# Kernel optimization log

Measured on AMD Instinct MI355X. Metric: run time of the kernel, lower is better.

Reference implementation:

```python
import jax, jax.numpy as jnp
import numpy as np

N_NODES = 100000
N_EDGES = 1600000
N_FEAT = 128
HIDDEN = 128
N_GRAPHS = 100


def setup_inputs() -> dict:
    key = jax.random.key(0)
    ks = jax.random.split(key, 12)
    glorot = lambda k, fi, fo: jax.random.normal(k, (fo, fi), jnp.float32) * (1.0 / np.sqrt(fi))
    x = jax.random.normal(ks[0], (N_NODES, N_FEAT), jnp.float32)
    edge_index = jax.random.randint(ks[1], (2, N_EDGES), 0, N_NODES, jnp.int64)
    batch = jnp.sort(jax.random.randint(ks[2], (N_NODES,), 0, N_GRAPHS, jnp.int64))
    return {
        "x": x,
        "edge_index": edge_index,
        "batch": batch,
        "W1": glorot(ks[3], N_FEAT, HIDDEN), "b1": jnp.zeros((HIDDEN,), jnp.float32),
        "W2": glorot(ks[4], HIDDEN, HIDDEN), "b2": jnp.zeros((HIDDEN,), jnp.float32),
        "W3": glorot(ks[5], HIDDEN, HIDDEN), "b3": jnp.zeros((HIDDEN,), jnp.float32),
        "W4": glorot(ks[6], HIDDEN, HIDDEN), "b4": jnp.zeros((HIDDEN,), jnp.float32),
    }


def _aggregate(x, edge_index):
    # GIN aggregation with eps=0: (1+eps)*x_i + sum_{j in N(i)} x_j
    src, dst = edge_index[0], edge_index[1]
    agg = jax.ops.segment_sum(x[src], dst, num_segments=N_NODES)
    return x + agg


def _mlp(h, Wa, ba, Wb, bb):
    h = jax.nn.relu(h @ Wa.T + ba)
    return jax.nn.relu(h @ Wb.T + bb)


def reference(x, edge_index, batch, W1, b1, W2, b2, W3, b3, W4, b4):
    # conv1: GINConv(MLP1), then extra relu (no-op after MLP's relu), dropout in eval = identity
    h = _mlp(_aggregate(x, edge_index), W1, b1, W2, b2)
    # conv2: GINConv(MLP2), then relu
    h = _mlp(_aggregate(h, edge_index), W3, b3, W4, b4)
    # global mean pool over graphs
    sums = jax.ops.segment_sum(h, batch, num_segments=N_GRAPHS)
    counts = jax.ops.segment_sum(jnp.ones((h.shape[0],), h.dtype), batch, num_segments=N_GRAPHS)
    x_pool = sums / jnp.maximum(counts, 1.0)[:, None]
    return (x_pool, h)
```

## Files before the change

### kernel.cpp

```cpp
#include <hip/hip_runtime.h>

#define N_NODES  100000
#define N_EDGES  1600000
#define NF       128
#define N_GRAPHS 100
#define NBKT     391
#define BKT_SHIFT 8
#define CAP      6144
#define CAPN     48
#define EPB      2048
#define EB_GRID  782
#define MBLK64   1563

typedef __attribute__((ext_vector_type(8))) short bf16x8;
typedef __attribute__((ext_vector_type(4))) float f32x4;
typedef __attribute__((ext_vector_type(2))) float f32x2;
typedef unsigned int uint32;

__device__ __forceinline__ unsigned short f2bf(float f) {
    union { float f; uint32 u; } x; x.f = f;
    return (unsigned short)((x.u + 0x7fffu + ((x.u >> 16) & 1u)) >> 16);
}
__device__ __forceinline__ uint32 pack2bf(float a, float b) {
    union { float f; uint32 u; } x, y; x.f = a; y.f = b;
    uint32 lo = (x.u + 0x7fffu + ((x.u >> 16) & 1u)) >> 16;
    uint32 hi = (y.u + 0x7fffu + ((y.u >> 16) & 1u)) & 0xffff0000u;
    return lo | hi;
}
__device__ __forceinline__ void add8(f32x2* acc, uint4 u4) {
    uint32 u[4] = {u4.x, u4.y, u4.z, u4.w};
    #pragma unroll
    for (int i = 0; i < 4; ++i) {
        union { uint32 b; float f; } lo, hi;
        lo.b = u[i] << 16; hi.b = u[i] & 0xffff0000u;
        acc[i] += (f32x2){lo.f, hi.f};
    }
}

__global__ __launch_bounds__(256) void prep(const float4* __restrict__ x,
                                            const float4* __restrict__ w1,
                                            const float4* __restrict__ w2,
                                            const float4* __restrict__ w3,
                                            const float4* __restrict__ w4,
                                            uint4* __restrict__ xb, uint4* __restrict__ wb,
                                            int* __restrict__ cur, float* __restrict__ sums) {
    int bid = blockIdx.x, t = threadIdx.x;
    if (bid < 6250) {
        int i = bid * 256 + t;
        float4 a = x[i * 2], b = x[i * 2 + 1];
        uint4 o;
        o.x = pack2bf(a.x, a.y); o.y = pack2bf(a.z, a.w);
        o.z = pack2bf(b.x, b.y); o.w = pack2bf(b.z, b.w);
        xb[i] = o;
    } else if (bid < 6282) {
        int i = (bid - 6250) * 256 + t;
        int wi = i >> 11, li = i & 2047;
        const float4* s = (wi == 0) ? w1 : (wi == 1) ? w2 : (wi == 2) ? w3 : w4;
        float4 a = s[li * 2], b = s[li * 2 + 1];
        uint4 o;
        o.x = pack2bf(a.x, a.y); o.y = pack2bf(a.z, a.w);
        o.z = pack2bf(b.x, b.y); o.w = pack2bf(b.z, b.w);
        wb[i] = o;
    } else {
        int idx = (bid - 6282) * 256 + t;
        for (int i = idx; i < N_GRAPHS * NF; i += 4096) sums[i] = 0.f;
        if (idx < NBKT) cur[idx] = 0;
    }
}

__global__ __launch_bounds__(512) void bscatter(const int* __restrict__ src,
                                                const int* __restrict__ dst,
                                                int* __restrict__ cur,
                                                uint32* __restrict__ ebuf) {
    __shared__ int lh[NBKT], lbase[NBKT];
    int t = threadIdx.x;
    if (t < NBKT) lh[t] = 0;
    __syncthreads();
    int e0 = blockIdx.x * EPB;
    int d[4];
    #pragma unroll
    for (int i = 0; i < 4; ++i) {
        int e = e0 + i * 512 + t;
        d[i] = -1;
        if (e < N_EDGES) { d[i] = dst[e]; atomicAdd(&lh[d[i] >> BKT_SHIFT], 1); }
    }
    __syncthreads();
    if (t < NBKT) { lbase[t] = t * CAP + (lh[t] ? atomicAdd(&cur[t], lh[t]) : 0); lh[t] = 0; }
    __syncthreads();
    #pragma unroll
    for (int i = 0; i < 4; ++i) {
        int e = e0 + i * 512 + t;
        if (e < N_EDGES) {
            int b = d[i] >> BKT_SHIFT;
            int off = atomicAdd(&lh[b], 1);
            ebuf[lbase[b] + off] = ((uint32)(d[i] & 255) << 17) | (uint32)src[e];
        }
    }
}

__global__ __launch_bounds__(256) void bfine(const uint32* __restrict__ ebuf,
                                             const int* __restrict__ cur,
                                             int* __restrict__ cnt,
                                             int* __restrict__ csr) {
    __shared__ int off[256];
    __shared__ __align__(16) int lcsr[256 * CAPN];
    int t = threadIdx.x;
    int bkt = blockIdx.x;
    int beg = bkt * CAP;
    int end = beg + min(cur[bkt], CAP);
    off[t] = 0;
    __syncthreads();
    for (int e = beg + t; e < end; e += 256) {
        uint32 u = ebuf[e];
        int local = (int)(u >> 17);
        int pos = atomicAdd(&off[local], 1);
        if (pos < CAPN)
            lcsr[local * CAPN + pos] = (int)(u & 0x1FFFFu);
    }
    __syncthreads();
    int node = (bkt << BKT_SHIFT) + t;
    if (node < N_NODES) cnt[node] = min(off[t], CAPN);
    uint4* dstq = (uint4*)(csr + (size_t)bkt * 256 * CAPN);
    const uint4* srcq = (const uint4*)lcsr;
    for (int i = t; i < 256 * CAPN / 4; i += 256)
        dstq[i] = srcq[i];
}

__global__ __launch_bounds__(256) void gather_agg_bf16(const uint4* __restrict__ x,
                                                       const int* __restrict__ cnt,
                                                       const int* __restrict__ csr,
                                                       uint4* __restrict__ out) {
    int gid  = blockIdx.x * 256 + threadIdx.x;
    int node = gid >> 6;
    int l = threadIdx.x & 63;
    int c = l & 15;
    int j = l >> 4;
    int beg = node * CAPN;

    uint4 vself = x[(size_t)node * 16 + c];
    int myE = csr[beg + min(l, CAPN - 1)];
    int deg = cnt[node];

    f32x2 acc[4];
    #pragma unroll
    for (int i = 0; i < 4; ++i) acc[i] = (f32x2){0.f, 0.f};

    uint4 v[8];
    int ok[8];
    #pragma unroll
    for (int k = 0; k < 4; ++k) {
        int sl = j + 4 * k;
        int sle = max(min(sl, deg - 1), 0);
        unsigned s = (unsigned)__shfl(myE, sle, 64);
        s = min(s, (unsigned)(N_NODES - 1));
        v[k] = x[(size_t)s * 16 + c];
        ok[k] = sl < deg;
    }
    if (deg > 16) {
        #pragma unroll
        for (int k = 0; k < 4; ++k) {
            int sl = 16 + j + 4 * k;
            int sle = min(sl, deg - 1);
            unsigned s = (unsigned)__shfl(myE, sle, 64);
            s = min(s, (unsigned)(N_NODES - 1));
            v[4 + k] = x[(size_t)s * 16 + c];
            ok[4 + k] = sl < deg;
        }
    }
    #pragma unroll
    for (int k = 0; k < 4; ++k) if (ok[k]) add8(acc, v[k]);
    if (deg > 16) {
        #pragma unroll
        for (int k = 0; k < 4; ++k) if (ok[4 + k]) add8(acc, v[4 + k]);
        for (int sl0 = 32; sl0 < deg; sl0 += 16) {
            #pragma unroll
            for (int k = 0; k < 4; ++k) {
                int sl = sl0 + j + 4 * k;
                int sle = min(sl, deg - 1);
                unsigned s = (unsigned)__shfl(myE, sle, 64);
                s = min(s, (unsigned)(N_NODES - 1));
                uint4 vv = x[(size_t)s * 16 + c];
                if (sl < deg) add8(acc, vv);
            }
        }
    }

    #pragma unroll
    for (int i = 0; i < 4; ++i) {
        acc[i].x += __shfl_xor(acc[i].x, 16, 64);
        acc[i].y += __shfl_xor(acc[i].y, 16, 64);
        acc[i].x += __shfl_xor(acc[i].x, 32, 64);
        acc[i].y += __shfl_xor(acc[i].y, 32, 64);
    }

    add8(acc, vself);

    if (j == 0) {
        uint4 o;
        o.x = pack2bf(acc[0].x, acc[0].y); o.y = pack2bf(acc[1].x, acc[1].y);
        o.z = pack2bf(acc[2].x, acc[2].y); o.w = pack2bf(acc[3].x, acc[3].y);
        out[(size_t)node * 16 + c] = o;
    }
}

template <bool F32OUT, bool POOL>
__global__ __launch_bounds__(256, 8) void mlp64(const unsigned short* __restrict__ A,
                                                const unsigned short* __restrict__ Wa,
                                                const float* __restrict__ ba,
                                                const unsigned short* __restrict__ Wb,
                                                const float* __restrict__ bb,
                                                void* __restrict__ Cout,
                                                const int* __restrict__ batch,
                                                float* __restrict__ sums) {
    __shared__ __align__(16) unsigned short Mid[64 * 136];
    int tid = threadIdx.x;
    int wv = tid >> 6, l = tid & 63, lm = l & 15, q = l >> 4;
    int row0  = blockIdx.x * 64;
    int trow0 = row0 + wv * 16;

    const unsigned short* pa  = A + (size_t)min(trow0 + lm, N_NODES - 1) * NF;
    const unsigned short* pwa = Wa + lm * NF;
    const unsigned short* pwb = Wb + lm * NF;

    f32x4 acc[8];
    #pragma unroll
    for (int ct = 0; ct < 8; ++ct) acc[ct] = (f32x4){0.f, 0.f, 0.f, 0.f};

    #pragma unroll
    for (int ks = 0; ks < 4; ++ks) {
        int ko = ks * 32 + q * 8;
        bf16x8 a = *(const bf16x8*)(pa + ko);
        #pragma unroll
        for (int ct = 0; ct < 8; ++ct) {
            bf16x8 b = *(const bf16x8*)(pwa + ct * 16 * NF + ko);
            acc[ct] = __builtin_amdgcn_mfma_f32_16x16x32_bf16(a, b, acc[ct], 0, 0, 0);
        }
    }

    #pragma unroll
    for (int ct = 0; ct < 8; ++ct) {
        int col = ct * 16 + lm;
        float bv = ba[col];
        #pragma unroll
        for (int r = 0; r < 4; ++r) {
            int rr = wv * 16 + q * 4 + r;
            Mid[rr * 136 + col] = f2bf(fmaxf(acc[ct][r] + bv, 0.f));
        }
    }
    __syncthreads();

    #pragma unroll
    for (int ct = 0; ct < 8; ++ct) acc[ct] = (f32x4){0.f, 0.f, 0.f, 0.f};

    const unsigned short* pm = &Mid[(wv * 16 + lm) * 136];
    #pragma unroll
    for (int ks = 0; ks < 4; ++ks) {
        int ko = ks * 32 + q * 8;
        bf16x8 a = *(const bf16x8*)(pm + ko);
        #pragma unroll
        for (int ct = 0; ct < 8; ++ct) {
            bf16x8 b = *(const bf16x8*)(pwb + ct * 16 * NF + ko);
            acc[ct] = __builtin_amdgcn_mfma_f32_16x16x32_bf16(a, b, acc[ct], 0, 0, 0);
        }
    }

    int gr[4];
    bool uni = true;
    if (POOL) {
        int gA = batch[min(trow0,      N_NODES - 1)];
        int gB = batch[min(trow0 + 15, N_NODES - 1)];
        uni = (gA == gB);
        gr[0] = gA;
        if (!uni) {
            #pragma unroll
            for (int r = 0; r < 4; ++r)
                gr[r] = batch[min(trow0 + q * 4 + r, N_NODES - 1)];
        }
    }

    #pragma unroll
    for (int ct = 0; ct < 8; ++ct) {
        int col = ct * 16 + lm;
        float bv = bb[col];
        float ps = 0.f;
        #pragma unroll
        for (int r = 0; r < 4; ++r) {
            int row = trow0 + q * 4 + r;
            if (row < N_NODES) {
                float vv = fmaxf(acc[ct][r] + bv, 0.f);
                if (F32OUT) ((float*)Cout)[(size_t)row * NF + col] = vv;
                else ((unsigned short*)Cout)[(size_t)row * NF + col] = f2bf(vv);
                if (POOL) {
                    if (uni) ps += vv;
                    else atomicAdd(&sums[gr[r] * NF + col], vv);
                }
            }
        }
        if (POOL && uni) {
            ps += __shfl_xor(ps, 16, 64);
            ps += __shfl_xor(ps, 32, 64);
            if (q == 0) atomicAdd(&sums[gr[0] * NF + col], ps);
        }
    }
}

__global__ __launch_bounds__(256) void pool_div2(const float* __restrict__ sums,
                                                 const int* __restrict__ batch,
                                                 float* __restrict__ out) {
    int i = blockIdx.x * 256 + threadIdx.x;
    if (i >= N_GRAPHS * NF) return;
    int g = i >> 7;
    int lo = 0, hi = N_NODES;
    while (lo < hi) { int m = (lo + hi) >> 1; if (batch[m] < g) lo = m + 1; else hi = m; }
    int lo2 = lo, hi2 = N_NODES;
    while (lo2 < hi2) { int m = (lo2 + hi2) >> 1; if (batch[m] < g + 1) lo2 = m + 1; else hi2 = m; }
    float cnt = (float)(lo2 - lo);
    out[i] = sums[i] / fmaxf(cnt, 1.f);
}

extern "C" void kernel_launch(void* const* d_in, const int* in_sizes, int n_in,
                              void* d_out, int out_size, void* d_ws, size_t ws_size,
                              hipStream_t stream) {
    const float* x     = (const float*)d_in[0];
    const int*   ei    = (const int*)d_in[1];
    const int*   batch = (const int*)d_in[2];
    const float* W1 = (const float*)d_in[3];  const float* b1 = (const float*)d_in[4];
    const float* W2 = (const float*)d_in[5];  const float* b2 = (const float*)d_in[6];
    const float* W3 = (const float*)d_in[7];  const float* b3 = (const float*)d_in[8];
    const float* W4 = (const float*)d_in[9];  const float* b4 = (const float*)d_in[10];
    const int* src = ei;
    const int* dst = ei + N_EDGES;

    float* out   = (float*)d_out;
    float* h_out = out + N_GRAPHS * NF;

    const size_t NE = (size_t)N_NODES * NF;
    unsigned short* xb = (unsigned short*)d_ws;
    unsigned short* t0 = xb + NE;
    unsigned short* t1 = t0 + NE;
    unsigned short* Wb = t1 + NE;
    int*    csr  = (int*)(Wb + 4 * NF * NF);
    int*    cntp = csr + (size_t)NBKT * 256 * CAPN;
    int*    curp = cntp + N_NODES;
    float*  sums = (float*)(curp + NBKT);
    uint32* ebuf = (uint32*)t1;

    const int gather_blocks = N_NODES * 64 / 256;

    prep<<<6250 + 32 + 16, 256, 0, stream>>>((const float4*)x,
                                             (const float4*)W1, (const float4*)W2,
                                             (const float4*)W3, (const float4*)W4,
                                             (uint4*)xb, (uint4*)Wb, curp, sums);

    bscatter<<<EB_GRID, 512, 0, stream>>>(src, dst, curp, ebuf);
    bfine<<<NBKT, 256, 0, stream>>>(ebuf, curp, cntp, csr);

    gather_agg_bf16<<<gather_blocks, 256, 0, stream>>>((const uint4*)xb, cntp, csr, (uint4*)t0);
    mlp64<false, false><<<MBLK64, 256, 0, stream>>>(t0, Wb + 0 * NF * NF, b1,
                                                    Wb + 1 * NF * NF, b2, t1, batch, sums);

    gather_agg_bf16<<<gather_blocks, 256, 0, stream>>>((const uint4*)t1, cntp, csr, (uint4*)t0);
    mlp64<true, true><<<MBLK64, 256, 0, stream>>>(t0, Wb + 2 * NF * NF, b3,
                                                  Wb + 3 * NF * NF, b4, h_out, batch, sums);

    pool_div2<<<(N_GRAPHS * NF + 255) / 256, 256, 0, stream>>>(sums, batch, out);
}
```

Measured before the change: 439.4 us.

## Double MLP row tile to 128 and stage outputs through LDS for coalesced stores

The fused two-layer MLP kernel now processes 128 rows per block: each wave computes two 16-row tiles and reuses each weight fragment load across both. The epilogue writes results into shared memory and then emits coalesced 16-byte row stores, instead of scattered per-element 2- or 4-byte stores. The fp32 output path is staged in two halves to fit in LDS. Costs are more registers and LDS, launch bounds reduced to 4 blocks, half as many blocks, and extra barriers.

```diff
diff --git a/kernel.cpp b/kernel.cpp
--- a/kernel.cpp
+++ b/kernel.cpp
@@ -10,7 +10,7 @@
 #define CAPN     48
 #define EPB      2048
 #define EB_GRID  782
-#define MBLK64   1563
+#define MBLK     782
 
 typedef __attribute__((ext_vector_type(8))) short bf16x8;
 typedef __attribute__((ext_vector_type(4))) float f32x4;
@@ -204,102 +204,153 @@
 }
 
 template <bool F32OUT, bool POOL>
-__global__ __launch_bounds__(256, 8) void mlp64(const unsigned short* __restrict__ A,
-                                                const unsigned short* __restrict__ Wa,
-                                                const float* __restrict__ ba,
-                                                const unsigned short* __restrict__ Wb,
-                                                const float* __restrict__ bb,
-                                                void* __restrict__ Cout,
-                                                const int* __restrict__ batch,
-                                                float* __restrict__ sums) {
-    __shared__ __align__(16) unsigned short Mid[64 * 136];
-    int tid = threadIdx.x;
+__global__ __launch_bounds__(256, 4) void mlp_mfma(const unsigned short* __restrict__ A,
+                                                   const unsigned short* __restrict__ Wa,
+                                                   const float* __restrict__ ba,
+                                                   const unsigned short* __restrict__ Wb,
+                                                   const float* __restrict__ bb,
+                                                   void* __restrict__ Cout,
+                                                   const int* __restrict__ batch,
+                                                   float* __restrict__ sums) {
+    __shared__ __align__(16) unsigned short Mid[128 * 136];
+    int tid  = threadIdx.x;
+    int row0 = blockIdx.x * 128;
     int wv = tid >> 6, l = tid & 63, lm = l & 15, q = l >> 4;
-    int row0  = blockIdx.x * 64;
-    int trow0 = row0 + wv * 16;
-
-    const unsigned short* pa  = A + (size_t)min(trow0 + lm, N_NODES - 1) * NF;
+
+    const unsigned short* pa0 = A + (size_t)min(row0 + wv * 32 + lm,      N_NODES - 1) * NF;
+    const unsigned short* pa1 = A + (size_t)min(row0 + wv * 32 + 16 + lm, N_NODES - 1) * NF;
     const unsigned short* pwa = Wa + lm * NF;
     const unsigned short* pwb = Wb + lm * NF;
 
-    f32x4 acc[8];
-    #pragma unroll
-    for (int ct = 0; ct < 8; ++ct) acc[ct] = (f32x4){0.f, 0.f, 0.f, 0.f};
+    f32x4 acc[2][8];
+    #pragma unroll
+    for (int i = 0; i < 2; ++i)
+        #pragma unroll
+        for (int j = 0; j < 8; ++j) acc[i][j] = (f32x4){0.f, 0.f, 0.f, 0.f};
 
     #pragma unroll
     for (int ks = 0; ks < 4; ++ks) {
         int ko = ks * 32 + q * 8;
-        bf16x8 a = *(const bf16x8*)(pa + ko);
+        bf16x8 a0 = *(const bf16x8*)(pa0 + ko);
+        bf16x8 a1 = *(const bf16x8*)(pa1 + ko);
         #pragma unroll
         for (int ct = 0; ct < 8; ++ct) {
             bf16x8 b = *(const bf16x8*)(pwa + ct * 16 * NF + ko);
-            acc[ct] = __builtin_amdgcn_mfma_f32_16x16x32_bf16(a, b, acc[ct], 0, 0, 0);
-        }
-    }
-
-    #pragma unroll
-    for (int ct = 0; ct < 8; ++ct) {
-        int col = ct * 16 + lm;
-        float bv = ba[col];
-        #pragma unroll
-        for (int r = 0; r < 4; ++r) {
-            int rr = wv * 16 + q * 4 + r;
-            Mid[rr * 136 + col] = f2bf(fmaxf(acc[ct][r] + bv, 0.f));
-        }
-    }
-    __syncthreads();
-
-    #pragma unroll
-    for (int ct = 0; ct < 8; ++ct) acc[ct] = (f32x4){0.f, 0.f, 0.f, 0.f};
-
-    const unsigned short* pm = &Mid[(wv * 16 + lm) * 136];
+            acc[0][ct] = __builtin_amdgcn_mfma_f32_16x16x32_bf16(a0, b, acc[0][ct], 0, 0, 0);
+            acc[1][ct] = __builtin_amdgcn_mfma_f32_16x16x32_bf16(a1, b, acc[1][ct], 0, 0, 0);
+        }
+    }
+
+    #pragma unroll
+    for (int rt = 0; rt < 2; ++rt)
+        #pragma unroll
+        for (int ct = 0; ct < 8; ++ct) {
+            int col = ct * 16 + lm;
+            float bv = ba[col];
+            #pragma unroll
+            for (int r = 0; r < 4; ++r) {
+                int rr = wv * 32 + rt * 16 + q * 4 + r;
+                Mid[rr * 136 + col] = f2bf(fmaxf(acc[rt][ct][r] + bv, 0.f));
+            }
+        }
+    __syncthreads();
+
+    #pragma unroll
+    for (int i = 0; i < 2; ++i)
+        #pragma unroll
+        for (int j = 0; j < 8; ++j) acc[i][j] = (f32x4){0.f, 0.f, 0.f, 0.f};
+
+    const unsigned short* pm0 = &Mid[(wv * 32 + lm) * 136];
+    const unsigned short* pm1 = &Mid[(wv * 32 + 16 + lm) * 136];
     #pragma unroll
     for (int ks = 0; ks < 4; ++ks) {
         int ko = ks * 32 + q * 8;
-        bf16x8 a = *(const bf16x8*)(pm + ko);
+        bf16x8 a0 = *(const bf16x8*)(pm0 + ko);
+        bf16x8 a1 = *(const bf16x8*)(pm1 + ko);
         #pragma unroll
         for (int ct = 0; ct < 8; ++ct) {
             bf16x8 b = *(const bf16x8*)(pwb + ct * 16 * NF + ko);
-            acc[ct] = __builtin_amdgcn_mfma_f32_16x16x32_bf16(a, b, acc[ct], 0, 0, 0);
-        }
-    }
-
-    int gr[4];
-    bool uni = true;
+            acc[0][ct] = __builtin_amdgcn_mfma_f32_16x16x32_bf16(a0, b, acc[0][ct], 0, 0, 0);
+            acc[1][ct] = __builtin_amdgcn_mfma_f32_16x16x32_bf16(a1, b, acc[1][ct], 0, 0, 0);
+        }
+    }
+    __syncthreads();
+
     if (POOL) {
-        int gA = batch[min(trow0,      N_NODES - 1)];
-        int gB = batch[min(trow0 + 15, N_NODES - 1)];
-        uni = (gA == gB);
-        gr[0] = gA;
-        if (!uni) {
+        #pragma unroll
+        for (int rt = 0; rt < 2; ++rt) {
+            int trow0 = row0 + wv * 32 + rt * 16;
+            int gA = batch[min(trow0,      N_NODES - 1)];
+            int gB = batch[min(trow0 + 15, N_NODES - 1)];
+            bool uni = (gA == gB);
             #pragma unroll
-            for (int r = 0; r < 4; ++r)
-                gr[r] = batch[min(trow0 + q * 4 + r, N_NODES - 1)];
-        }
-    }
-
-    #pragma unroll
-    for (int ct = 0; ct < 8; ++ct) {
-        int col = ct * 16 + lm;
-        float bv = bb[col];
-        float ps = 0.f;
-        #pragma unroll
-        for (int r = 0; r < 4; ++r) {
-            int row = trow0 + q * 4 + r;
-            if (row < N_NODES) {
-                float vv = fmaxf(acc[ct][r] + bv, 0.f);
-                if (F32OUT) ((float*)Cout)[(size_t)row * NF + col] = vv;
-                else ((unsigned short*)Cout)[(size_t)row * NF + col] = f2bf(vv);
-                if (POOL) {
-                    if (uni) ps += vv;
-                    else atomicAdd(&sums[gr[r] * NF + col], vv);
+            for (int ct = 0; ct < 8; ++ct) {
+                int col = ct * 16 + lm;
+                float bv = bb[col];
+                float ps = 0.f;
+                #pragma unroll
+                for (int r = 0; r < 4; ++r) {
+                    int row = trow0 + q * 4 + r;
+                    if (row < N_NODES) {
+                        float vv = fmaxf(acc[rt][ct][r] + bv, 0.f);
+                        if (uni) ps += vv;
+                        else atomicAdd(&sums[batch[row] * NF + col], vv);
+                    }
                 }
-            }
-        }
-        if (POOL && uni) {
-            ps += __shfl_xor(ps, 16, 64);
-            ps += __shfl_xor(ps, 32, 64);
-            if (q == 0) atomicAdd(&sums[gr[0] * NF + col], ps);
+                if (uni) {
+                    ps += __shfl_xor(ps, 16, 64);
+                    ps += __shfl_xor(ps, 32, 64);
+                    if (q == 0) atomicAdd(&sums[gA * NF + col], ps);
+                }
+            }
+        }
+    }
+
+    if (!F32OUT) {
+        #pragma unroll
+        for (int rt = 0; rt < 2; ++rt)
+            #pragma unroll
+            for (int ct = 0; ct < 8; ++ct) {
+                int col = ct * 16 + lm;
+                float bv = bb[col];
+                #pragma unroll
+                for (int r = 0; r < 4; ++r) {
+                    int rr = wv * 32 + rt * 16 + q * 4 + r;
+                    Mid[rr * 136 + col] = f2bf(fmaxf(acc[rt][ct][r] + bv, 0.f));
+                }
+            }
+        __syncthreads();
+        for (int i = tid; i < 128 * 16; i += 256) {
+            int row = i >> 4, c = i & 15;
+            if (row0 + row < N_NODES)
+                ((uint4*)Cout)[(size_t)(row0 + row) * 16 + c] = *(const uint4*)&Mid[row * 136 + c * 8];
+        }
+    } else {
+        float* Mf = (float*)Mid;
+        #pragma unroll
+        for (int h = 0; h < 2; ++h) {
+            if ((wv >> 1) == h) {
+                #pragma unroll
+                for (int rt = 0; rt < 2; ++rt)
+                    #pragma unroll
+                    for (int ct = 0; ct < 8; ++ct) {
+                        int col = ct * 16 + lm;
+                        float bv = bb[col];
+                        #pragma unroll
+                        for (int r = 0; r < 4; ++r) {
+                            int lr = (wv & 1) * 32 + rt * 16 + q * 4 + r;
+                            Mf[lr * 132 + col] = fmaxf(acc[rt][ct][r] + bv, 0.f);
+                        }
+                    }
+            }
+            __syncthreads();
+            for (int i = tid; i < 64 * 32; i += 256) {
+                int lr = i >> 5, c = i & 31;
+                int row = row0 + h * 64 + lr;
+                if (row < N_NODES)
+                    ((float4*)Cout)[(size_t)row * 32 + c] = *(const float4*)&Mf[lr * 132 + c * 4];
+            }
+            __syncthreads();
         }
     }
 }
@@ -356,12 +407,12 @@
     bfine<<<NBKT, 256, 0, stream>>>(ebuf, curp, cntp, csr);
 
     gather_agg_bf16<<<gather_blocks, 256, 0, stream>>>((const uint4*)xb, cntp, csr, (uint4*)t0);
-    mlp64<false, false><<<MBLK64, 256, 0, stream>>>(t0, Wb + 0 * NF * NF, b1,
-                                                    Wb + 1 * NF * NF, b2, t1, batch, sums);
+    mlp_mfma<false, false><<<MBLK, 256, 0, stream>>>(t0, Wb + 0 * NF * NF, b1,
+                                                     Wb + 1 * NF * NF, b2, t1, batch, sums);
 
     gather_agg_bf16<<<gather_blocks, 256, 0, stream>>>((const uint4*)t1, cntp, csr, (uint4*)t0);
-    mlp64<true, true><<<MBLK64, 256, 0, stream>>>(t0, Wb + 2 * NF * NF, b3,
-                                                  Wb + 3 * NF * NF, b4, h_out, batch, sums);
+    mlp_mfma<true, true><<<MBLK, 256, 0, stream>>>(t0, Wb + 2 * NF * NF, b3,
+                                                   Wb + 3 * NF * NF, b4, h_out, batch, sums);
 
     pool_div2<<<(N_GRAPHS * NF + 255) / 256, 256, 0, stream>>>(sums, batch, out);
 }
```

New measurement: 388.0 us. 1.13x faster.
